# Optimization experiments

Measured on AMD Instinct MI355X. Metric: run time of the kernel, lower is better.

## Reference

```python
import jax, jax.numpy as jnp
import numpy as np

CUTOFF = 5.0
N_RBF = 50
N_INTER = 6
B = 1024          # molecules per batch
N_PER_MOL = 32    # atoms per molecule
MAX_Z = 100
D = 128           # n_atom_basis == n_filters == head_hidden


def _ssp(x):
    # schnetpack shifted softplus activation
    return jax.nn.softplus(x) - jnp.log(2.0).astype(x.dtype)


def setup_inputs() -> dict:
    key = jax.random.key(0)
    ks = jax.random.split(key, 18)
    total = B * N_PER_MOL
    atomic_numbers = jax.random.randint(ks[0], (total,), 1, MAX_Z, dtype=jnp.int32)
    positions = jax.random.uniform(ks[1], (total, 3), dtype=jnp.float32) * 10.0
    # all ordered intra-molecule pairs with i != j; pairs beyond the cutoff are
    # zeroed by the cosine cutoff factor, matching the torch neighbor-list math
    loc = np.arange(N_PER_MOL)
    ii, jj = np.meshgrid(loc, loc, indexing='ij')
    m = ii != jj
    li, lj = ii[m], jj[m]                      # [n*(n-1)]
    off = (np.arange(B) * N_PER_MOL)[:, None]
    idx_i = jnp.asarray((off + li[None, :]).reshape(-1), dtype=jnp.int32)
    idx_j = jnp.asarray((off + lj[None, :]).reshape(-1), dtype=jnp.int32)
    batch_idx = jnp.asarray(np.repeat(np.arange(B), N_PER_MOL), dtype=jnp.int32)
    n_atoms = jnp.full((B,), N_PER_MOL, dtype=jnp.int32)
    s = 0.05
    emb = jax.random.normal(ks[2], (MAX_Z, D), jnp.float32) * s
    Wi  = jax.random.normal(ks[3], (N_INTER, D, D), jnp.float32) * s      # in2f (no bias)
    Wf1 = jax.random.normal(ks[4], (N_INTER, N_RBF, D), jnp.float32) * s  # filter net
    bf1 = jax.random.normal(ks[5], (N_INTER, D), jnp.float32) * s
    Wf2 = jax.random.normal(ks[6], (N_INTER, D, D), jnp.float32) * s
    bf2 = jax.random.normal(ks[7], (N_INTER, D), jnp.float32) * s
    Wo1 = jax.random.normal(ks[8], (N_INTER, D, D), jnp.float32) * s      # f2out
    bo1 = jax.random.normal(ks[9], (N_INTER, D), jnp.float32) * s
    Wo2 = jax.random.normal(ks[10], (N_INTER, D, D), jnp.float32) * s
    bo2 = jax.random.normal(ks[11], (N_INTER, D), jnp.float32) * s
    Wh1 = jax.random.normal(ks[12], (D, D), jnp.float32) * s              # MLP head
    bh1 = jax.random.normal(ks[13], (D,), jnp.float32) * s
    Wh2 = jax.random.normal(ks[14], (D, 1), jnp.float32) * s
    bh2 = jax.random.normal(ks[15], (1,), jnp.float32) * s
    return dict(atomic_numbers=atomic_numbers, positions=positions, idx_i=idx_i,
                idx_j=idx_j, batch_idx=batch_idx, n_atoms=n_atoms, emb=emb,
                Wi=Wi, Wf1=Wf1, bf1=bf1, Wf2=Wf2, bf2=bf2,
                Wo1=Wo1, bo1=bo1, Wo2=Wo2, bo2=bo2,
                Wh1=Wh1, bh1=bh1, Wh2=Wh2, bh2=bh2)


def reference(atomic_numbers, positions, idx_i, idx_j, batch_idx, n_atoms,
              emb, Wi, Wf1, bf1, Wf2, bf2, Wo1, bo1, Wo2, bo2,
              Wh1, bh1, Wh2, bh2):
    total = atomic_numbers.shape[0]
    nmol = n_atoms.shape[0]
    # pairwise displacement / distance over neighbor list
    Rij = positions[idx_j] - positions[idx_i]                    # [P,3]
    d = jnp.sqrt(jnp.sum(Rij * Rij, axis=-1))                    # [P]
    # GaussianRBF: centers on [0, cutoff], width = spacing
    centers = jnp.linspace(0.0, CUTOFF, N_RBF, dtype=d.dtype)
    width = CUTOFF / (N_RBF - 1)
    coeff = -0.5 / (width * width)
    f_ij = jnp.exp(coeff * (d[:, None] - centers[None, :]) ** 2)  # [P,R]
    # CosineCutoff (zero beyond cutoff -> out-of-range pairs contribute nothing)
    rcut = 0.5 * (jnp.cos(d * jnp.pi / CUTOFF) + 1.0) * (d < CUTOFF)  # [P]
    x = emb[atomic_numbers]                                       # [N,D]
    for l in range(N_INTER):
        W = _ssp(f_ij @ Wf1[l] + bf1[l]) @ Wf2[l] + bf2[l]        # [P,D] filters
        W = W * rcut[:, None]
        xf = x @ Wi[l]                                            # in2f, no bias
        msg = xf[idx_j] * W                                       # gather + modulate
        agg = jax.ops.segment_sum(msg, idx_i, num_segments=total) # scatter-add
        v = _ssp(agg @ Wo1[l] + bo1[l]) @ Wo2[l] + bo2[l]         # f2out
        x = x + v                                                 # residual
    mol = jax.ops.segment_sum(x, batch_idx, num_segments=nmol)    # sum pooling
    h = jax.nn.silu(mol @ Wh1 + bh1)
    pred = (h @ Wh2 + bh2)[:, 0]                                  # squeeze(-1)
    return pred
```

## Files before the change

kernel.cpp:

```cpp
#include <hip/hip_runtime.h>
#include <math.h>

#define TOTAL  32768
#define NMOL   1024
#define NA     32
#define DIM    128
#define NRBF   50
#define NLAYER 6

typedef __attribute__((ext_vector_type(16))) float f32x16;
typedef _Float16 h2 __attribute__((ext_vector_type(2)));
typedef __fp16 hf8 __attribute__((ext_vector_type(8)));

#define OFF_TAB 0
#define OFF_WA  0
#define OFF_POS 33792
#define OFF_XB  34816
#define OFF_AGG 34816
#define OFF_XF  52224
#define OFF_CM  69632
#define OFF_AM  73600
#define LDS_TOTAL 81536

#define WS_WIT   0
#define WS_WO1T  208896
#define WS_WO2T  417792
#define WS_TAB   655360

#define KSTEP  0.10204081632653061f
#define C1     -48.0200005f
#define NTAB   192
#define TSCALE 38.200000763f

__device__ __forceinline__ unsigned pk2_f16(float lo, float hi) {
  return __builtin_bit_cast(unsigned, __builtin_amdgcn_cvt_pkrtz(lo, hi));
}
__device__ __forceinline__ float ssp_f(float v) {
  float e = __expf(-fabsf(v));
  return fmaxf(v, 0.0f) + __logf(1.0f + e) - 0.69314718055994531f;
}
__device__ __forceinline__ hf8 ldsH(const char* p) {
  return __builtin_bit_cast(hf8, *reinterpret_cast<const uint4*>(p));
}
__device__ __forceinline__ int inv_partner(int r, int i) {
  if (i == 31) return r;
  int mm = i - r; if (mm < 0) mm += 31;
  if (mm == 0) return 31;
  int jj = 2 * r - i; jj %= 31; if (jj < 0) jj += 31;
  return jj;
}

__global__ void k_prep(const float* __restrict__ Wi, const float* __restrict__ Wo1,
                       const float* __restrict__ Wo2, short* __restrict__ ws) {
  const int kind = blockIdx.y, l = blockIdx.z;
  const int idx = blockIdx.x * 256 + threadIdx.x;
  int c = idx / 136, kp = idx % 136;
  const float* s = (kind == 0) ? Wi : (kind == 1) ? Wo1 : Wo2;
  size_t base = (kind == 0) ? WS_WIT : (kind == 1) ? WS_WO1T : WS_WO2T;
  float v = (kp < 128) ? s[(size_t)l * DIM * DIM + kp * DIM + c] : 0.0f;
  ws[base / 2 + (size_t)l * 128 * 136 + idx] =
      (short)__builtin_bit_cast(unsigned short, (_Float16)v);
}

__global__ void k_tab(const float* __restrict__ Wf1, const float* __restrict__ bf1,
                      const float* __restrict__ Wf2, const float* __restrict__ bf2,
                      short* __restrict__ tab) {
  __shared__ float fs[64];
  __shared__ float hs[128];
  const int g = blockIdx.x, l = blockIdx.y, c = threadIdx.x;
  const float d = (float)g * (5.0f / 191.0f);
  if (c < NRBF) { float tt = d - (float)c * KSTEP; fs[c] = __expf(C1 * tt * tt); }
  __syncthreads();
  float h = bf1[l * DIM + c];
#pragma unroll 5
  for (int k = 0; k < NRBF; ++k) h += fs[k] * Wf1[((size_t)l * NRBF + k) * DIM + c];
  hs[c] = ssp_f(h);
  __syncthreads();
  float wv = bf2[l * DIM + c];
#pragma unroll 8
  for (int k = 0; k < DIM; ++k) wv += hs[k] * Wf2[((size_t)l * DIM + k) * DIM + c];
  tab[((size_t)l * NTAB + g) * 136 + c] =
      (short)__builtin_bit_cast(unsigned short, (_Float16)wv);
}

__global__ __launch_bounds__(512, 4) void k_fused(
    const int* __restrict__ z, const float* __restrict__ pos,
    const float* __restrict__ emb,
    const short* __restrict__ wiT, const short* __restrict__ wo1T,
    const short* __restrict__ wo2T, const short* __restrict__ tabA,
    const float* __restrict__ bo1, const float* __restrict__ bo2,
    const float* __restrict__ Wh1, const float* __restrict__ bh1,
    const float* __restrict__ Wh2, const float* __restrict__ bh2,
    float* __restrict__ out) {
  extern __shared__ char sm[];
  const int t = threadIdx.x;
  const int bid = blockIdx.x;
  const int w = t >> 6, lane = t & 63, hl = lane >> 5, lr = lane & 31;
  const int m = w >> 2, wl = w & 3;
  const int ai = t & 31;
  const int acg = (t >> 5) & 7;
  const int cgo = acg * 16;

  char*  wA  = sm + OFF_WA;
  char*  XBm = sm + OFF_XB + m * 8704;
  char*  XFm = sm + OFF_XF + m * 8704;
  char*  AGm = sm + OFF_AGG + m * 8704;
  float* VXf = (float*)(sm + 0);
  float* poss = (float*)(sm + OFF_POS);
  const unsigned short* cmm = (const unsigned short*)(sm + OFF_CM) + m * 992;
  const unsigned* amm = (const unsigned*)(sm + OFF_AM) + m * 992;

  if (t < 192) poss[t] = pos[(size_t)bid * 192 + t];
  __syncthreads();
  for (int u = t; u < 2048; u += 512) {
    int m2 = u >> 10, e = u & 1023;
    if (e < 992) {
      int r = e >> 5, i = e & 31;
      int j = inv_partner(r, i);
      const float* pm = poss + m2 * 96;
      float dx = pm[j * 3 + 0] - pm[i * 3 + 0];
      float dy = pm[j * 3 + 1] - pm[i * 3 + 1];
      float dz = pm[j * 3 + 2] - pm[i * 3 + 2];
      float d = sqrtf(dx * dx + dy * dy + dz * dz);
      float rc = 0.5f * (__cosf(d * 0.62831853071795865f) + 1.0f);
      rc = (d < 5.0f) ? rc : 0.0f;
      float u0 = fminf(d * TSCALE, 190.0f);
      int g = (int)u0;
      float f = u0 - (float)g;
      ((unsigned short*)(sm + OFF_CM))[m2 * 992 + e] =
          (unsigned short)(((unsigned)g << 5) | (unsigned)j);
      ((unsigned*)(sm + OFF_AM))[m2 * 992 + e] = pk2_f16((1.0f - f) * rc, f * rc);
    }
  }
  float xr[16];
  {
    const float* er = emb + (size_t)z[(bid * 2 + m) * NA + ai] * DIM;
    float4 e0 = *(const float4*)&er[acg * 8];
    float4 e1 = *(const float4*)&er[acg * 8 + 4];
    float4 e2 = *(const float4*)&er[64 + acg * 8];
    float4 e3 = *(const float4*)&er[64 + acg * 8 + 4];
    xr[0] = e0.x; xr[1] = e0.y; xr[2]  = e0.z; xr[3]  = e0.w;
    xr[4] = e1.x; xr[5] = e1.y; xr[6]  = e1.z; xr[7]  = e1.w;
    xr[8] = e2.x; xr[9] = e2.y; xr[10] = e2.z; xr[11] = e2.w;
    xr[12] = e3.x; xr[13] = e3.y; xr[14] = e3.z; xr[15] = e3.w;
  }
  __syncthreads();

  for (int l = 0; l < NLAYER; ++l) {
    const short* wiL  = wiT  + (size_t)l * 17408;
    const short* wo1L = wo1T + (size_t)l * 17408;
    const short* wo2L = wo2T + (size_t)l * 17408;
    const short* tabL = tabA + (size_t)l * NTAB * 136;
    const float bo1r = bo1[l * DIM + wl * 32 + lr];
    const float bo2r = bo2[l * DIM + wl * 32 + lr];

    {
      uint4 s0, s1;
      s0.x = pk2_f16(xr[0], xr[1]);   s0.y = pk2_f16(xr[2], xr[3]);
      s0.z = pk2_f16(xr[4], xr[5]);   s0.w = pk2_f16(xr[6], xr[7]);
      s1.x = pk2_f16(xr[8], xr[9]);   s1.y = pk2_f16(xr[10], xr[11]);
      s1.z = pk2_f16(xr[12], xr[13]); s1.w = pk2_f16(xr[14], xr[15]);
      *(uint4*)(XBm + ai * 272 + cgo) = s0;
      *(uint4*)(XBm + ai * 272 + cgo + 128) = s1;
    }
    for (int u = t; u < 2176; u += 512) ((uint4*)wA)[u] = ((const uint4*)wiL)[u];
    __syncthreads();

    {
      f32x16 acc;
#pragma unroll
      for (int q = 0; q < 16; ++q) acc[q] = 0.0f;
      const int col = wl * 32 + lr;
#pragma unroll
      for (int ks = 0; ks < 8; ++ks) {
        hf8 a = ldsH(XBm + lr * 272 + ks * 32 + hl * 16);
        hf8 b = ldsH(wA + col * 272 + ks * 32 + hl * 16);
        acc = __builtin_amdgcn_mfma_f32_32x32x16_f16(a, b, acc, 0, 0, 0);
      }
#pragma unroll
      for (int rg = 0; rg < 16; rg += 2) {
        int row = (rg & 3) + 8 * (rg >> 2) + 4 * hl;
        unsigned pk = pk2_f16(acc[rg], acc[rg + 1]);
        *(unsigned short*)(XFm + row * 272 + col * 2) = (unsigned short)pk;
        *(unsigned short*)(XFm + (row + 1) * 272 + col * 2) = (unsigned short)(pk >> 16);
      }
    }
    __syncthreads();

    for (int u = t; u < 3264; u += 512) ((uint4*)(sm + OFF_TAB))[u] = ((const uint4*)tabL)[u];
    __syncthreads();

    h2 acc_h[8];
#pragma unroll
    for (int q = 0; q < 8; ++q) acc_h[q] = (h2)(_Float16)0.0f;
#pragma unroll 4
    for (int r = 0; r < 31; ++r) {
      unsigned e = cmm[(r << 5) + ai];
      unsigned a = amm[(r << 5) + ai];
      int foff = (int)(e & 31u) * 272;
      int gboff = (int)(e >> 5) * 272;
      h2 a00h = __builtin_bit_cast(h2, __builtin_amdgcn_perm(a, a, 0x01000100u));
      h2 a11h = __builtin_bit_cast(h2, __builtin_amdgcn_perm(a, a, 0x03020302u));
      const char* tp = sm + OFF_TAB + gboff + cgo;
      uint4 T00 = *(const uint4*)(tp);
      uint4 T01 = *(const uint4*)(tp + 128);
      uint4 T10 = *(const uint4*)(tp + 272);
      uint4 T11 = *(const uint4*)(tp + 400);
      const char* fp = XFm + foff + cgo;
      uint4 F0 = *(const uint4*)(fp);
      uint4 F1 = *(const uint4*)(fp + 128);
#define AGCH(q, t0u, t1u, fu)                                        \
      { h2 wv = a00h * __builtin_bit_cast(h2, t0u)                   \
              + a11h * __builtin_bit_cast(h2, t1u);                  \
        acc_h[q] = wv * __builtin_bit_cast(h2, fu) + acc_h[q]; }
      AGCH(0, T00.x, T10.x, F0.x)
      AGCH(1, T00.y, T10.y, F0.y)
      AGCH(2, T00.z, T10.z, F0.z)
      AGCH(3, T00.w, T10.w, F0.w)
      AGCH(4, T01.x, T11.x, F1.x)
      AGCH(5, T01.y, T11.y, F1.y)
      AGCH(6, T01.z, T11.z, F1.z)
      AGCH(7, T01.w, T11.w, F1.w)
#undef AGCH
    }
    __syncthreads();

    {
      uint4 s0, s1;
      s0.x = __builtin_bit_cast(unsigned, acc_h[0]);
      s0.y = __builtin_bit_cast(unsigned, acc_h[1]);
      s0.z = __builtin_bit_cast(unsigned, acc_h[2]);
      s0.w = __builtin_bit_cast(unsigned, acc_h[3]);
      s1.x = __builtin_bit_cast(unsigned, acc_h[4]);
      s1.y = __builtin_bit_cast(unsigned, acc_h[5]);
      s1.z = __builtin_bit_cast(unsigned, acc_h[6]);
      s1.w = __builtin_bit_cast(unsigned, acc_h[7]);
      *(uint4*)(AGm + ai * 272 + cgo) = s0;
      *(uint4*)(AGm + ai * 272 + cgo + 128) = s1;
    }
    for (int u = t; u < 2176; u += 512) ((uint4*)wA)[u] = ((const uint4*)wo1L)[u];
    __syncthreads();

    float t1v[16];
    {
      f32x16 acc;
#pragma unroll
      for (int q = 0; q < 16; ++q) acc[q] = 0.0f;
      const int col = wl * 32 + lr;
#pragma unroll
      for (int ks = 0; ks < 8; ++ks) {
        hf8 a = ldsH(AGm + lr * 272 + ks * 32 + hl * 16);
        hf8 b = ldsH(wA + col * 272 + ks * 32 + hl * 16);
        acc = __builtin_amdgcn_mfma_f32_32x32x16_f16(a, b, acc, 0, 0, 0);
      }
#pragma unroll
      for (int rg = 0; rg < 16; ++rg) t1v[rg] = ssp_f(acc[rg] + bo1r);
    }
    __syncthreads();
    {
      const int col = wl * 32 + lr;
#pragma unroll
      for (int rg = 0; rg < 16; rg += 2) {
        int row = (rg & 3) + 8 * (rg >> 2) + 4 * hl;
        unsigned pk = pk2_f16(t1v[rg], t1v[rg + 1]);
        *(unsigned short*)(AGm + row * 272 + col * 2) = (unsigned short)pk;
        *(unsigned short*)(AGm + (row + 1) * 272 + col * 2) = (unsigned short)(pk >> 16);
      }
    }
    for (int u = t; u < 2176; u += 512) ((uint4*)wA)[u] = ((const uint4*)wo2L)[u];
    __syncthreads();

    {
      f32x16 acc;
#pragma unroll
      for (int q = 0; q < 16; ++q) acc[q] = 0.0f;
      const int col = wl * 32 + lr;
#pragma unroll
      for (int ks = 0; ks < 8; ++ks) {
        hf8 a = ldsH(AGm + lr * 272 + ks * 32 + hl * 16);
        hf8 b = ldsH(wA + col * 272 + ks * 32 + hl * 16);
        acc = __builtin_amdgcn_mfma_f32_32x32x16_f16(a, b, acc, 0, 0, 0);
      }
      __syncthreads();
#pragma unroll
      for (int rg = 0; rg < 16; ++rg) {
        int row = (rg & 3) + 8 * (rg >> 2) + 4 * hl;
        VXf[m * 4224 + row * 132 + col] = acc[rg] + bo2r;
      }
    }
    __syncthreads();
    {
      const float* vp = VXf + m * 4224 + ai * 132;
      float4 v0 = *(const float4*)&vp[acg * 8];
      float4 v1 = *(const float4*)&vp[acg * 8 + 4];
      float4 v2 = *(const float4*)&vp[64 + acg * 8];
      float4 v3 = *(const float4*)&vp[64 + acg * 8 + 4];
      xr[0] += v0.x; xr[1] += v0.y; xr[2]  += v0.z; xr[3]  += v0.w;
      xr[4] += v1.x; xr[5] += v1.y; xr[6]  += v1.z; xr[7]  += v1.w;
      xr[8] += v2.x; xr[9] += v2.y; xr[10] += v2.z; xr[11] += v2.w;
      xr[12] += v3.x; xr[13] += v3.y; xr[14] += v3.z; xr[15] += v3.w;
    }
    __syncthreads();
  }

#pragma unroll
  for (int off = 1; off < 32; off <<= 1) {
#pragma unroll
    for (int q = 0; q < 16; ++q) xr[q] += __shfl_xor(xr[q], off);
  }
  float* molS = (float*)(sm + 0);
  float* hsum = (float*)(sm + 2048);
  if (ai == 0) {
#pragma unroll
    for (int q = 0; q < 8; ++q) molS[m * 132 + acg * 8 + q] = xr[q];
#pragma unroll
    for (int q = 0; q < 8; ++q) molS[m * 132 + 64 + acg * 8 + q] = xr[8 + q];
  }
  __syncthreads();
  if (t < 256) {
    int mm = t >> 7, c = t & 127;
    float h = bh1[c];
#pragma unroll 8
    for (int k = 0; k < 128; ++k) h += molS[mm * 132 + k] * Wh1[k * 128 + c];
    h = h / (1.0f + __expf(-h));
    hsum[mm * 128 + c] = h * Wh2[c];
  }
  for (int off = 64; off > 0; off >>= 1) {
    __syncthreads();
    if (t < 256) {
      int mm = t >> 7, c = t & 127;
      if (c < off) hsum[mm * 128 + c] += hsum[mm * 128 + c + off];
    }
  }
  __syncthreads();
  if (t < 2) out[bid * 2 + t] = hsum[t * 128] + bh2[0];
}

extern "C" void kernel_launch(void* const* d_in, const int* in_sizes, int n_in,
                              void* d_out, int out_size, void* d_ws, size_t ws_size,
                              hipStream_t stream) {
  const int*   z    = (const int*)d_in[0];
  const float* pos  = (const float*)d_in[1];
  const float* emb  = (const float*)d_in[6];
  const float* Wi   = (const float*)d_in[7];
  const float* Wf1  = (const float*)d_in[8];
  const float* bf1  = (const float*)d_in[9];
  const float* Wf2  = (const float*)d_in[10];
  const float* bf2  = (const float*)d_in[11];
  const float* Wo1  = (const float*)d_in[12];
  const float* bo1  = (const float*)d_in[13];
  const float* Wo2  = (const float*)d_in[14];
  const float* bo2  = (const float*)d_in[15];
  const float* Wh1  = (const float*)d_in[16];
  const float* bh1  = (const float*)d_in[17];
  const float* Wh2  = (const float*)d_in[18];
  const float* bh2  = (const float*)d_in[19];
  float* out = (float*)d_out;

  short* wsS = (short*)d_ws;
  const short* wiT  = wsS + WS_WIT  / 2;
  const short* wo1T = wsS + WS_WO1T / 2;
  const short* wo2T = wsS + WS_WO2T / 2;
  const short* tab  = wsS + WS_TAB  / 2;

  (void)hipFuncSetAttribute(reinterpret_cast<const void*>(k_fused),
                            hipFuncAttributeMaxDynamicSharedMemorySize, LDS_TOTAL);

  k_prep<<<dim3(68, 3, 6), 256, 0, stream>>>(Wi, Wo1, Wo2, wsS);
  k_tab<<<dim3(NTAB, 6), 128, 0, stream>>>(Wf1, bf1, Wf2, bf2, wsS + WS_TAB / 2);
  k_fused<<<NMOL / 2, 512, LDS_TOTAL, stream>>>(
      z, pos, emb, wiT, wo1T, wo2T, tab, bo1, bo2, Wh1, bh1, Wh2, bh2, out);
}
```

Measured before the change: 132.5 us.

## Prefetch next-stage weights into registers and fold residual update into XF buffer

Global loads of the next weight matrix or filter table are issued into registers one phase early, so their latency overlaps the current MFMA or aggregation phase. The LDS store then happens after the barrier, replacing the synchronous copy loops. The f2out result is now written to the XF buffer as fp16 and added to the residual at the start of the next layer, which removes a float staging buffer and two barriers per layer. The trade-off is higher register pressure from the prefetch registers and fp16 rounding of the residual delta.

After: 126.9 us. 4.2% less time.

```diff
diff --git a/kernel.cpp b/kernel.cpp
--- a/kernel.cpp
+++ b/kernel.cpp
@@ -105,7 +105,6 @@
   char*  XBm = sm + OFF_XB + m * 8704;
   char*  XFm = sm + OFF_XF + m * 8704;
   char*  AGm = sm + OFF_AGG + m * 8704;
-  float* VXf = (float*)(sm + 0);
   float* poss = (float*)(sm + OFF_POS);
   const unsigned short* cmm = (const unsigned short*)(sm + OFF_CM) + m * 992;
   const unsigned* amm = (const unsigned*)(sm + OFF_AM) + m * 992;
@@ -144,16 +143,38 @@
     xr[8] = e2.x; xr[9] = e2.y; xr[10] = e2.z; xr[11] = e2.w;
     xr[12] = e3.x; xr[13] = e3.y; xr[14] = e3.z; xr[15] = e3.w;
   }
-  __syncthreads();
+  uint4 pw0, pw1, pw2, pw3, pw4;
+  {
+    const uint4* s4 = (const uint4*)wiT;
+    pw0 = s4[t]; pw1 = s4[t + 512]; pw2 = s4[t + 1024]; pw3 = s4[t + 1536];
+    if (t < 128) pw4 = s4[t + 2048];
+  }
+  __syncthreads();
+
+  uint4 pq0, pq1, pq2, pq3, pq4;
+  uint4 pt0, pt1, pt2, pt3, pt4, pt5, pt6;
 
   for (int l = 0; l < NLAYER; ++l) {
-    const short* wiL  = wiT  + (size_t)l * 17408;
-    const short* wo1L = wo1T + (size_t)l * 17408;
-    const short* wo2L = wo2T + (size_t)l * 17408;
     const short* tabL = tabA + (size_t)l * NTAB * 136;
     const float bo1r = bo1[l * DIM + wl * 32 + lr];
     const float bo2r = bo2[l * DIM + wl * 32 + lr];
 
+    ((uint4*)wA)[t] = pw0; ((uint4*)wA)[t + 512] = pw1;
+    ((uint4*)wA)[t + 1024] = pw2; ((uint4*)wA)[t + 1536] = pw3;
+    if (t < 128) ((uint4*)wA)[t + 2048] = pw4;
+    if (l > 0) {
+      uint4 v0 = *(const uint4*)(XFm + ai * 272 + cgo);
+      uint4 v1 = *(const uint4*)(XFm + ai * 272 + cgo + 128);
+      h2 hv;
+      hv = __builtin_bit_cast(h2, v0.x); xr[0]  += (float)hv[0]; xr[1]  += (float)hv[1];
+      hv = __builtin_bit_cast(h2, v0.y); xr[2]  += (float)hv[0]; xr[3]  += (float)hv[1];
+      hv = __builtin_bit_cast(h2, v0.z); xr[4]  += (float)hv[0]; xr[5]  += (float)hv[1];
+      hv = __builtin_bit_cast(h2, v0.w); xr[6]  += (float)hv[0]; xr[7]  += (float)hv[1];
+      hv = __builtin_bit_cast(h2, v1.x); xr[8]  += (float)hv[0]; xr[9]  += (float)hv[1];
+      hv = __builtin_bit_cast(h2, v1.y); xr[10] += (float)hv[0]; xr[11] += (float)hv[1];
+      hv = __builtin_bit_cast(h2, v1.z); xr[12] += (float)hv[0]; xr[13] += (float)hv[1];
+      hv = __builtin_bit_cast(h2, v1.w); xr[14] += (float)hv[0]; xr[15] += (float)hv[1];
+    }
     {
       uint4 s0, s1;
       s0.x = pk2_f16(xr[0], xr[1]);   s0.y = pk2_f16(xr[2], xr[3]);
@@ -163,7 +184,12 @@
       *(uint4*)(XBm + ai * 272 + cgo) = s0;
       *(uint4*)(XBm + ai * 272 + cgo + 128) = s1;
     }
-    for (int u = t; u < 2176; u += 512) ((uint4*)wA)[u] = ((const uint4*)wiL)[u];
+    {
+      const uint4* s4 = (const uint4*)tabL;
+      pt0 = s4[t]; pt1 = s4[t + 512]; pt2 = s4[t + 1024];
+      pt3 = s4[t + 1536]; pt4 = s4[t + 2048]; pt5 = s4[t + 2560];
+      if (t < 192) pt6 = s4[t + 3072];
+    }
     __syncthreads();
 
     {
@@ -187,7 +213,18 @@
     }
     __syncthreads();
 
-    for (int u = t; u < 3264; u += 512) ((uint4*)(sm + OFF_TAB))[u] = ((const uint4*)tabL)[u];
+    ((uint4*)(sm + OFF_TAB))[t] = pt0;
+    ((uint4*)(sm + OFF_TAB))[t + 512] = pt1;
+    ((uint4*)(sm + OFF_TAB))[t + 1024] = pt2;
+    ((uint4*)(sm + OFF_TAB))[t + 1536] = pt3;
+    ((uint4*)(sm + OFF_TAB))[t + 2048] = pt4;
+    ((uint4*)(sm + OFF_TAB))[t + 2560] = pt5;
+    if (t < 192) ((uint4*)(sm + OFF_TAB))[t + 3072] = pt6;
+    {
+      const uint4* s4 = (const uint4*)(wo1T + (size_t)l * 17408);
+      pq0 = s4[t]; pq1 = s4[t + 512]; pq2 = s4[t + 1024]; pq3 = s4[t + 1536];
+      if (t < 128) pq4 = s4[t + 2048];
+    }
     __syncthreads();
 
     h2 acc_h[8];
@@ -238,7 +275,14 @@
       *(uint4*)(AGm + ai * 272 + cgo) = s0;
       *(uint4*)(AGm + ai * 272 + cgo + 128) = s1;
     }
-    for (int u = t; u < 2176; u += 512) ((uint4*)wA)[u] = ((const uint4*)wo1L)[u];
+    ((uint4*)wA)[t] = pq0; ((uint4*)wA)[t + 512] = pq1;
+    ((uint4*)wA)[t + 1024] = pq2; ((uint4*)wA)[t + 1536] = pq3;
+    if (t < 128) ((uint4*)wA)[t + 2048] = pq4;
+    {
+      const uint4* s4 = (const uint4*)(wo2T + (size_t)l * 17408);
+      pw0 = s4[t]; pw1 = s4[t + 512]; pw2 = s4[t + 1024]; pw3 = s4[t + 1536];
+      if (t < 128) pw4 = s4[t + 2048];
+    }
     __syncthreads();
 
     float t1v[16];
@@ -257,6 +301,7 @@
       for (int rg = 0; rg < 16; ++rg) t1v[rg] = ssp_f(acc[rg] + bo1r);
     }
     __syncthreads();
+
     {
       const int col = wl * 32 + lr;
 #pragma unroll
@@ -267,10 +312,18 @@
         *(unsigned short*)(AGm + (row + 1) * 272 + col * 2) = (unsigned short)(pk >> 16);
       }
     }
-    for (int u = t; u < 2176; u += 512) ((uint4*)wA)[u] = ((const uint4*)wo2L)[u];
-    __syncthreads();
-
-    {
+    ((uint4*)wA)[t] = pw0; ((uint4*)wA)[t + 512] = pw1;
+    ((uint4*)wA)[t + 1024] = pw2; ((uint4*)wA)[t + 1536] = pw3;
+    if (t < 128) ((uint4*)wA)[t + 2048] = pw4;
+    __syncthreads();
+
+    {
+      {
+        const short* wiN = wiT + (size_t)((l + 1 < NLAYER) ? (l + 1) : l) * 17408;
+        const uint4* s4 = (const uint4*)wiN;
+        pw0 = s4[t]; pw1 = s4[t + 512]; pw2 = s4[t + 1024]; pw3 = s4[t + 1536];
+        if (t < 128) pw4 = s4[t + 2048];
+      }
       f32x16 acc;
 #pragma unroll
       for (int q = 0; q < 16; ++q) acc[q] = 0.0f;
@@ -281,26 +334,29 @@
         hf8 b = ldsH(wA + col * 272 + ks * 32 + hl * 16);
         acc = __builtin_amdgcn_mfma_f32_32x32x16_f16(a, b, acc, 0, 0, 0);
       }
-      __syncthreads();
-#pragma unroll
-      for (int rg = 0; rg < 16; ++rg) {
+#pragma unroll
+      for (int rg = 0; rg < 16; rg += 2) {
         int row = (rg & 3) + 8 * (rg >> 2) + 4 * hl;
-        VXf[m * 4224 + row * 132 + col] = acc[rg] + bo2r;
-      }
-    }
-    __syncthreads();
-    {
-      const float* vp = VXf + m * 4224 + ai * 132;
-      float4 v0 = *(const float4*)&vp[acg * 8];
-      float4 v1 = *(const float4*)&vp[acg * 8 + 4];
-      float4 v2 = *(const float4*)&vp[64 + acg * 8];
-      float4 v3 = *(const float4*)&vp[64 + acg * 8 + 4];
-      xr[0] += v0.x; xr[1] += v0.y; xr[2]  += v0.z; xr[3]  += v0.w;
-      xr[4] += v1.x; xr[5] += v1.y; xr[6]  += v1.z; xr[7]  += v1.w;
-      xr[8] += v2.x; xr[9] += v2.y; xr[10] += v2.z; xr[11] += v2.w;
-      xr[12] += v3.x; xr[13] += v3.y; xr[14] += v3.z; xr[15] += v3.w;
-    }
-    __syncthreads();
+        unsigned pk = pk2_f16(acc[rg] + bo2r, acc[rg + 1] + bo2r);
+        *(unsigned short*)(XFm + row * 272 + col * 2) = (unsigned short)pk;
+        *(unsigned short*)(XFm + (row + 1) * 272 + col * 2) = (unsigned short)(pk >> 16);
+      }
+    }
+    __syncthreads();
+  }
+
+  {
+    uint4 v0 = *(const uint4*)(XFm + ai * 272 + cgo);
+    uint4 v1 = *(const uint4*)(XFm + ai * 272 + cgo + 128);
+    h2 hv;
+    hv = __builtin_bit_cast(h2, v0.x); xr[0]  += (float)hv[0]; xr[1]  += (float)hv[1];
+    hv = __builtin_bit_cast(h2, v0.y); xr[2]  += (float)hv[0]; xr[3]  += (float)hv[1];
+    hv = __builtin_bit_cast(h2, v0.z); xr[4]  += (float)hv[0]; xr[5]  += (float)hv[1];
+    hv = __builtin_bit_cast(h2, v0.w); xr[6]  += (float)hv[0]; xr[7]  += (float)hv[1];
+    hv = __builtin_bit_cast(h2, v1.x); xr[8]  += (float)hv[0]; xr[9]  += (float)hv[1];
+    hv = __builtin_bit_cast(h2, v1.y); xr[10] += (float)hv[0]; xr[11] += (float)hv[1];
+    hv = __builtin_bit_cast(h2, v1.z); xr[12] += (float)hv[0]; xr[13] += (float)hv[1];
+    hv = __builtin_bit_cast(h2, v1.w); xr[14] += (float)hv[0]; xr[15] += (float)hv[1];
   }
 
 #pragma unroll
```
